# Optimization experiments

Measured on AMD Instinct MI355X. Metric: run time of the kernel, lower is better.

The kernel has to match this reference:

```python
import jax, jax.numpy as jnp
import numpy as np

N_EMBD = 1024

def setup_inputs() -> dict:
    key = jax.random.key(0)
    ks = jax.random.split(key, 7)
    x = jax.random.normal(ks[0], (4, 2048, N_EMBD), dtype=jnp.float32)
    s = 1.0 / np.sqrt(N_EMBD)
    Wk = jax.random.normal(ks[1], (N_EMBD, N_EMBD), dtype=jnp.float32) * s
    bk = jnp.zeros((N_EMBD,), dtype=jnp.float32)
    Wq = jax.random.normal(ks[2], (N_EMBD, N_EMBD), dtype=jnp.float32) * s
    bq = jnp.zeros((N_EMBD,), dtype=jnp.float32)
    Wv = jax.random.normal(ks[3], (N_EMBD, N_EMBD), dtype=jnp.float32) * s
    bv = jnp.zeros((N_EMBD,), dtype=jnp.float32)
    return {"x": x, "Wk": Wk, "bk": bk, "Wq": Wq, "bq": bq, "Wv": Wv, "bv": bv}

def reference(x, Wk, bk, Wq, bq, Wv, bv):
    B, T, C = x.shape
    k = x @ Wk.T + bk  # [B,T,C]
    q = x @ Wq.T + bq
    v = x @ Wv.T + bv
    # scaled scores with causal mask (note: original scales by C**-0.5)
    scores = jnp.einsum('btc,bsc->bts', q, k) * (C ** -0.5)  # [B,T,T]
    causal = jnp.tril(jnp.ones((T, T), dtype=bool))
    scores = jnp.where(causal, scores, -jnp.inf)
    weights = jax.nn.softmax(scores, axis=-1)
    # dropout disabled (inference mode)
    y = jnp.einsum('bts,bsc->btc', weights, v)
    return y
```

## Files before the change

kernel.cpp:

```cpp
#include <hip/hip_runtime.h>
#include <hip/hip_bf16.h>

typedef __attribute__((ext_vector_type(8))) short short8;
typedef __attribute__((ext_vector_type(4))) float f32x4;

__device__ __forceinline__ ushort f2b(float f) {
    __hip_bfloat16 h = __float2bfloat16(f);
    return *reinterpret_cast<ushort*>(&h);
}
__device__ __forceinline__ float b2f(ushort u) {
    return __uint_as_float(((unsigned)u) << 16);
}
__device__ __forceinline__ void gload16(const ushort* g, ushort* l) {
    __builtin_amdgcn_global_load_lds(
        (const __attribute__((address_space(1))) void*)g,
        (__attribute__((address_space(3))) void*)l, 16, 0, 0);
}

__global__ __launch_bounds__(512, 1) void qkv_gemm256(
    const ushort* __restrict__ xb, const ushort* __restrict__ Wcat,
    const float* __restrict__ bk, const float* __restrict__ bq, const float* __restrict__ bv,
    ushort* __restrict__ Kb, ushort* __restrict__ Qb, ushort* __restrict__ Vt) {
    constexpr int T = 2048, C = 1024, K = 1024, NT = 16;
    __shared__ ushort smem[49152];

    const int tid = threadIdx.x;
    const int l = tid & 63, w = tid >> 6;
    const int wm = (w >> 2) * 128, wn = (w & 3) * 32;
    const int lr = l & 15, lk = l >> 4;

    const int b = blockIdx.x;
    const int wg = (b & 7) * 96 + (b >> 3);
    const int m0 = (wg / 24) * 256, n0 = (wg % 24) * 128;

    const int srow = w * 16 + (l >> 2);
    const int scb = ((l & 3) << 4) ^ ((l & 32) ? 32 : 0);
    const ushort* gA = xb + (size_t)(m0 + srow) * K + (scb >> 1);
    const ushort* gB = Wcat + (size_t)(n0 + srow) * K + (scb >> 1);

    const int LB = lr * 32 + ((lk << 3) ^ ((lr >= 8) ? 16 : 0));

    f32x4 acc[8][2] = {};

#define STAGEQ(u1, ks)                                                    \
    {                                                                     \
        ushort* _base = smem + ((u1) & 1) * 24576 + (ks) * 12288;         \
        const int _ko = (u1) * 64 + (ks) * 32;                            \
        ushort* _da = _base + w * 512;                                    \
        gload16(gA + _ko, _da);                                           \
        gload16(gA + (size_t)128 * K + _ko, _da + 4096);                  \
        gload16(gB + _ko, _base + 8192 + w * 512);                        \
    }

    STAGEQ(0, 0);
    STAGEQ(0, 1);

    for (int u = 0; u < NT; ++u) {
        const ushort* buf = smem + (u & 1) * 24576;
        asm volatile("s_waitcnt vmcnt(3)" ::: "memory");
        __builtin_amdgcn_s_barrier();
        asm volatile("" ::: "memory");
        {
            const ushort* Ab = buf + (wm >> 4) * 512 + LB;
            const ushort* Bb = buf + 8192 + (wn >> 4) * 512 + LB;
            short8 a[8], bf2[2];
#pragma unroll
            for (int f = 0; f < 8; ++f) a[f] = *reinterpret_cast<const short8*>(Ab + f * 512);
            bf2[0] = *reinterpret_cast<const short8*>(Bb);
            bf2[1] = *reinterpret_cast<const short8*>(Bb + 512);
            if (u + 1 < NT) STAGEQ(u + 1, 0);
            __builtin_amdgcn_s_setprio(1);
#pragma unroll
            for (int f = 0; f < 8; ++f)
#pragma unroll
                for (int g = 0; g < 2; ++g)
                    acc[f][g] = __builtin_amdgcn_mfma_f32_16x16x32_bf16(a[f], bf2[g], acc[f][g], 0, 0, 0);
            __builtin_amdgcn_s_setprio(0);
        }
        if (u + 1 < NT) asm volatile("s_waitcnt vmcnt(3)" ::: "memory");
        else            asm volatile("s_waitcnt vmcnt(0)" ::: "memory");
        __builtin_amdgcn_s_barrier();
        asm volatile("" ::: "memory");
        {
            const ushort* Ab = buf + 12288 + (wm >> 4) * 512 + LB;
            const ushort* Bb = buf + 12288 + 8192 + (wn >> 4) * 512 + LB;
            short8 a[8], bf2[2];
#pragma unroll
            for (int f = 0; f < 8; ++f) a[f] = *reinterpret_cast<const short8*>(Ab + f * 512);
            bf2[0] = *reinterpret_cast<const short8*>(Bb);
            bf2[1] = *reinterpret_cast<const short8*>(Bb + 512);
            if (u + 1 < NT) STAGEQ(u + 1, 1);
            __builtin_amdgcn_s_setprio(1);
#pragma unroll
            for (int f = 0; f < 8; ++f)
#pragma unroll
                for (int g = 0; g < 2; ++g)
                    acc[f][g] = __builtin_amdgcn_mfma_f32_16x16x32_bf16(a[f], bf2[g], acc[f][g], 0, 0, 0);
            __builtin_amdgcn_s_setprio(0);
        }
    }
#undef STAGEQ

    const int zsel = n0 >> 10;
    const int c0 = (n0 & 1023) + wn;
    if (zsel < 2) {
        ushort* O = (zsel == 0) ? Kb : Qb;
        const float* bias = (zsel == 0) ? bk : bq;
#pragma unroll
        for (int f = 0; f < 8; ++f)
#pragma unroll
            for (int g = 0; g < 2; ++g) {
                const int gc = c0 + g * 16 + lr;
                const float badd = bias[gc];
#pragma unroll
                for (int rr = 0; rr < 4; ++rr) {
                    const int gr = m0 + wm + f * 16 + lk * 4 + rr;
                    O[(size_t)gr * C + gc] = f2b(acc[f][g][rr] + badd);
                }
            }
    } else {
        const int zb = (m0 + wm) >> 11;
        const int s0 = (m0 + wm) & 2047;
        ushort* Vz = Vt + (size_t)zb * C * T;
#pragma unroll
        for (int f = 0; f < 8; ++f)
#pragma unroll
            for (int g = 0; g < 2; ++g) {
                const int gc = c0 + g * 16 + lr;
                const float badd = bv[gc];
                const int s = s0 + f * 16 + lk * 4;
                ushort tmp[4];
#pragma unroll
                for (int rr = 0; rr < 4; ++rr) tmp[rr] = f2b(acc[f][g][rr] + badd);
                *reinterpret_cast<uint2*>(Vz + (size_t)gc * T + s) =
                    *reinterpret_cast<uint2*>(tmp);
            }
    }
}

template <int MODE>
__global__ __launch_bounds__(256, 3) void gemm_ring(
    const ushort* __restrict__ Kb, const ushort* __restrict__ Qb,
    const ushort* __restrict__ Vt, ushort* __restrict__ Sb, float* __restrict__ out) {
    constexpr int T = 2048, C = 1024;
    __shared__ ushort smem[24576];

    const int tid = threadIdx.x;
    const int l = tid & 63, w = tid >> 6;
    const int wm = (w >> 1) * 64, wn = (w & 1) * 64;
    const int lr = l & 15, lk = l >> 4;

    int m0, n0, nt, iblk = 0, jblk = 0, z = 0;
    const ushort *Au, *Bu;
    int ldA, ldB;
    if constexpr (MODE == 1) {
        const int wg0 = blockIdx.x;
        const int wg = (wg0 & 7) * 68 + (wg0 >> 3);
        z = wg / 136; const int t136 = wg % 136;
        int i = (int)((sqrtf(8.f * t136 + 1.f) - 1.f) * 0.5f);
        while ((i + 1) * (i + 2) / 2 <= t136) ++i;
        while (i * (i + 1) / 2 > t136) --i;
        const int j = t136 - i * (i + 1) / 2;
        iblk = i; jblk = j;
        m0 = i * 128; n0 = j * 128;
        Au = Qb + (size_t)z * T * C + (size_t)m0 * C; ldA = C;
        Bu = Kb + (size_t)z * T * C + (size_t)n0 * C; ldB = C;
        nt = 32;
    } else {
        const int wg0 = blockIdx.x;
        const int wg = (wg0 & 7) * 64 + (wg0 >> 3);
        const int half = wg >> 8, s2 = wg & 255;
        z = s2 >> 6; const int r6 = s2 & 63;
        const int nb = r6 & 7, ii = r6 >> 3;
        const int i = half ? (15 - ii) : ii;
        iblk = i;
        m0 = i * 128; n0 = nb * 128;
        Au = Sb + (size_t)z * T * T + (size_t)m0 * T; ldA = T;
        Bu = Vt + (size_t)z * C * T + (size_t)n0 * T; ldB = T;
        nt = 4 * (i + 1);
    }

    const int srow = w * 16 + (l >> 2);
    const int scb = ((l & 3) << 4) ^ ((l >= 32) ? 32 : 0);
    const ushort* gA = Au + (size_t)srow * ldA + (scb >> 1);
    const ushort* gB = Bu + (size_t)srow * ldB + (scb >> 1);
    const size_t a64 = (size_t)64 * ldA, b64 = (size_t)64 * ldB;
    const int LBu = lr * 32 + ((lk << 3) ^ ((lr >= 8) ? 16 : 0));

    f32x4 acc[4][4] = {};

#define STAGE(tt, sl)                                                    \
    {                                                                    \
        const int _ko = (tt) * 32;                                       \
        ushort* _d = smem + (sl) * 8192 + w * 512;                       \
        gload16(gA + _ko,        _d);                                    \
        gload16(gA + a64 + _ko,  _d + 2048);                             \
        gload16(gB + _ko,        _d + 4096);                             \
        gload16(gB + b64 + _ko,  _d + 6144);                             \
    }

    STAGE(0, 0);
    STAGE(1, 1);
    asm volatile("s_waitcnt vmcnt(4)" ::: "memory");
    __builtin_amdgcn_s_barrier();
    asm volatile("" ::: "memory");

    int sc = 0, ss = 2;
    for (int t = 0; t < nt; ++t) {
        const ushort* As = smem + sc * 8192 + (wm >> 4) * 512 + LBu;
        const ushort* Bs = smem + sc * 8192 + 4096 + (wn >> 4) * 512 + LBu;
        short8 af[4], bf[4];
#pragma unroll
        for (int q = 0; q < 4; ++q) {
            af[q] = *reinterpret_cast<const short8*>(As + q * 512);
            bf[q] = *reinterpret_cast<const short8*>(Bs + q * 512);
        }
        if (t + 2 < nt) STAGE(t + 2, ss);
        __builtin_amdgcn_s_setprio(1);
#pragma unroll
        for (int mf = 0; mf < 4; ++mf)
#pragma unroll
            for (int nf = 0; nf < 4; ++nf)
                acc[mf][nf] = __builtin_amdgcn_mfma_f32_16x16x32_bf16(af[mf], bf[nf], acc[mf][nf], 0, 0, 0);
        __builtin_amdgcn_s_setprio(0);
        if (t + 1 < nt) {
            if (t + 2 < nt) asm volatile("s_waitcnt vmcnt(4)" ::: "memory");
            else            asm volatile("s_waitcnt vmcnt(0)" ::: "memory");
            __builtin_amdgcn_s_barrier();
            asm volatile("" ::: "memory");
        }
        sc = (sc == 2) ? 0 : sc + 1;
        ss = (ss == 2) ? 0 : ss + 1;
    }
#undef STAGE

    if constexpr (MODE == 1) {
        ushort* Sp = Sb + (size_t)z * T * T;
        const bool diag = (iblk == jblk);
#pragma unroll
        for (int mf = 0; mf < 4; ++mf)
#pragma unroll
            for (int nf = 0; nf < 4; ++nf) {
                const int gc = n0 + wn + nf * 16 + lr;
#pragma unroll
                for (int rr = 0; rr < 4; ++rr) {
                    const int gr = m0 + wm + mf * 16 + lk * 4 + rr;
                    if (!diag || gc <= gr)
                        Sp[(size_t)gr * T + gc] = f2b(acc[mf][nf][rr] * 0.03125f);
                }
            }
    } else {
        float* Op = out + (size_t)z * T * C;
#pragma unroll
        for (int mf = 0; mf < 4; ++mf)
#pragma unroll
            for (int nf = 0; nf < 4; ++nf) {
                const int gc = n0 + wn + nf * 16 + lr;
#pragma unroll
                for (int rr = 0; rr < 4; ++rr) {
                    const int gr = m0 + wm + mf * 16 + lk * 4 + rr;
                    Op[(size_t)gr * C + gc] = acc[mf][nf][rr];
                }
            }
    }
}

__global__ __launch_bounds__(256) void cvt_all(
    const float* __restrict__ x, const float* __restrict__ Wk,
    const float* __restrict__ Wq, const float* __restrict__ Wv,
    ushort* __restrict__ xb, ushort* __restrict__ Wcat) {
    constexpr int C = 1024;
    constexpr int NX = 8388608 / 8, NW = C * C / 8;
    int i = blockIdx.x * 256 + threadIdx.x;
    const float* src; ushort* dst;
    if (i < NX)               { src = x;  dst = xb; }
    else if (i < NX + NW)     { src = Wk; dst = Wcat;                 i -= NX; }
    else if (i < NX + 2 * NW) { src = Wq; dst = Wcat + (size_t)C * C; i -= NX + NW; }
    else                      { src = Wv; dst = Wcat + 2 * (size_t)C * C; i -= NX + 2 * NW; }
    const float4* p = reinterpret_cast<const float4*>(src) + (size_t)i * 2;
    float4 a = p[0], b = p[1];
    ushort o[8] = {f2b(a.x), f2b(a.y), f2b(a.z), f2b(a.w),
                   f2b(b.x), f2b(b.y), f2b(b.z), f2b(b.w)};
    reinterpret_cast<uint4*>(dst)[i] = *reinterpret_cast<uint4*>(o);
}

__global__ __launch_bounds__(256) void softmax_rows(ushort* __restrict__ S, int T) {
    const int g = blockIdx.x;
    const int r = g & (T - 1);
    ushort* p = S + (size_t)g * T;
    const int tid = threadIdx.x;
    const int lane = tid & 63, wave = tid >> 6;
    const int c0 = tid * 8;
    const int n_write = ((r >> 7) + 1) << 7;

    float f[8];
    if (c0 <= r) {
        uint4 raw = *reinterpret_cast<const uint4*>(p + c0);
        ushort* rs = reinterpret_cast<ushort*>(&raw);
#pragma unroll
        for (int j = 0; j < 8; ++j) f[j] = (c0 + j <= r) ? b2f(rs[j]) : -INFINITY;
    } else {
#pragma unroll
        for (int j = 0; j < 8; ++j) f[j] = -INFINITY;
    }

    float mx = f[0];
#pragma unroll
    for (int j = 1; j < 8; ++j) mx = fmaxf(mx, f[j]);
#pragma unroll
    for (int o = 32; o > 0; o >>= 1) mx = fmaxf(mx, __shfl_xor(mx, o));

    __shared__ float redm[4], reds[4];
    if (lane == 0) redm[wave] = mx;
    __syncthreads();
    mx = fmaxf(fmaxf(redm[0], redm[1]), fmaxf(redm[2], redm[3]));

    float e[8], s = 0.f;
#pragma unroll
    for (int j = 0; j < 8; ++j) { e[j] = __expf(f[j] - mx); s += e[j]; }
#pragma unroll
    for (int o = 32; o > 0; o >>= 1) s += __shfl_xor(s, o);
    if (lane == 0) reds[wave] = s;
    __syncthreads();
    s = reds[0] + reds[1] + reds[2] + reds[3];

    const float inv = 1.f / s;
    if (c0 < n_write) {
        ushort outv[8];
#pragma unroll
        for (int j = 0; j < 8; ++j) outv[j] = f2b(e[j] * inv);
        *reinterpret_cast<uint4*>(p + c0) = *reinterpret_cast<uint4*>(outv);
    }
}

extern "C" void kernel_launch(void* const* d_in, const int* in_sizes, int n_in,
                              void* d_out, int out_size, void* d_ws, size_t ws_size,
                              hipStream_t stream) {
    const float* x  = (const float*)d_in[0];
    const float* Wk = (const float*)d_in[1];
    const float* bk = (const float*)d_in[2];
    const float* Wq = (const float*)d_in[3];
    const float* bq = (const float*)d_in[4];
    const float* Wv = (const float*)d_in[5];
    const float* bv = (const float*)d_in[6];
    float* out = (float*)d_out;

    constexpr int B = 4, T = 2048, C = 1024;
    constexpr size_t BTC = (size_t)B * T * C;

    ushort* Kb = (ushort*)d_ws;
    ushort* Qb = Kb + BTC;
    ushort* Vt = Qb + BTC;
    ushort* Sb = Vt + BTC;
    ushort* xb   = Sb;
    ushort* Wcat = Sb + BTC;

    dim3 blk(256);

    cvt_all<<<dim3(5632), blk, 0, stream>>>(x, Wk, Wq, Wv, xb, Wcat);

    qkv_gemm256<<<dim3(768), dim3(512), 0, stream>>>(xb, Wcat, bk, bq, bv, Kb, Qb, Vt);

    gemm_ring<1><<<dim3(544), blk, 0, stream>>>(Kb, Qb, Vt, Sb, out);

    softmax_rows<<<dim3(B * T), blk, 0, stream>>>(Sb, T);

    gemm_ring<2><<<dim3(512), blk, 0, stream>>>(Kb, Qb, Vt, Sb, out);
}
```

Before: 145.6 us.

## Enlarge QKV GEMM tile to 256x256 with 4-slot k32 LDS ring

```diff
diff --git a/kernel.cpp b/kernel.cpp
--- a/kernel.cpp
+++ b/kernel.cpp
@@ -21,17 +21,17 @@
     const ushort* __restrict__ xb, const ushort* __restrict__ Wcat,
     const float* __restrict__ bk, const float* __restrict__ bq, const float* __restrict__ bv,
     ushort* __restrict__ Kb, ushort* __restrict__ Qb, ushort* __restrict__ Vt) {
-    constexpr int T = 2048, C = 1024, K = 1024, NT = 16;
-    __shared__ ushort smem[49152];
+    constexpr int T = 2048, C = 1024, K = 1024, NT = 32;
+    __shared__ ushort smem[65536];
 
     const int tid = threadIdx.x;
     const int l = tid & 63, w = tid >> 6;
-    const int wm = (w >> 2) * 128, wn = (w & 3) * 32;
+    const int wm = (w >> 2) * 128, wn = (w & 3) * 64;
     const int lr = l & 15, lk = l >> 4;
 
     const int b = blockIdx.x;
-    const int wg = (b & 7) * 96 + (b >> 3);
-    const int m0 = (wg / 24) * 256, n0 = (wg % 24) * 128;
+    const int wg = (b & 7) * 48 + (b >> 3);
+    const int m0 = (wg / 12) * 256, n0 = (wg % 12) * 256;
 
     const int srow = w * 16 + (l >> 2);
     const int scb = ((l & 3) << 4) ^ ((l & 32) ? 32 : 0);
@@ -39,65 +39,49 @@
     const ushort* gB = Wcat + (size_t)(n0 + srow) * K + (scb >> 1);
 
     const int LB = lr * 32 + ((lk << 3) ^ ((lr >= 8) ? 16 : 0));
-
-    f32x4 acc[8][2] = {};
-
-#define STAGEQ(u1, ks)                                                    \
+    const int Abase = (wm >> 7) * 4096;
+    const int Bbase = 8192 + ((wn >> 7) * 4096) + ((wn & 64) >> 4) * 512;
+
+    f32x4 acc[8][4] = {};
+
+#define STAGEQ(tt)                                                        \
     {                                                                     \
-        ushort* _base = smem + ((u1) & 1) * 24576 + (ks) * 12288;         \
-        const int _ko = (u1) * 64 + (ks) * 32;                            \
-        ushort* _da = _base + w * 512;                                    \
-        gload16(gA + _ko, _da);                                           \
-        gload16(gA + (size_t)128 * K + _ko, _da + 4096);                  \
-        gload16(gB + _ko, _base + 8192 + w * 512);                        \
-    }
-
-    STAGEQ(0, 0);
-    STAGEQ(0, 1);
+        const int _ko = (tt) * 32;                                        \
+        ushort* _s = smem + ((tt) & 3) * 16384 + w * 512;                 \
+        gload16(gA + _ko,                  _s);                           \
+        gload16(gA + (size_t)128 * K + _ko, _s + 4096);                   \
+        gload16(gB + _ko,                  _s + 8192);                    \
+        gload16(gB + (size_t)128 * K + _ko, _s + 12288);                  \
+    }
+
+    STAGEQ(0); STAGEQ(1); STAGEQ(2);
 
     for (int u = 0; u < NT; ++u) {
-        const ushort* buf = smem + (u & 1) * 24576;
-        asm volatile("s_waitcnt vmcnt(3)" ::: "memory");
+        const int rem = NT - 1 - u;
+        if (rem >= 2)      asm volatile("s_waitcnt vmcnt(8)" ::: "memory");
+        else if (rem == 1) asm volatile("s_waitcnt vmcnt(4)" ::: "memory");
+        else               asm volatile("s_waitcnt vmcnt(0)" ::: "memory");
         __builtin_amdgcn_s_barrier();
         asm volatile("" ::: "memory");
-        {
-            const ushort* Ab = buf + (wm >> 4) * 512 + LB;
-            const ushort* Bb = buf + 8192 + (wn >> 4) * 512 + LB;
-            short8 a[8], bf2[2];
-#pragma unroll
-            for (int f = 0; f < 8; ++f) a[f] = *reinterpret_cast<const short8*>(Ab + f * 512);
-            bf2[0] = *reinterpret_cast<const short8*>(Bb);
-            bf2[1] = *reinterpret_cast<const short8*>(Bb + 512);
-            if (u + 1 < NT) STAGEQ(u + 1, 0);
-            __builtin_amdgcn_s_setprio(1);
-#pragma unroll
-            for (int f = 0; f < 8; ++f)
-#pragma unroll
-                for (int g = 0; g < 2; ++g)
-                    acc[f][g] = __builtin_amdgcn_mfma_f32_16x16x32_bf16(a[f], bf2[g], acc[f][g], 0, 0, 0);
-            __builtin_amdgcn_s_setprio(0);
-        }
-        if (u + 1 < NT) asm volatile("s_waitcnt vmcnt(3)" ::: "memory");
-        else            asm volatile("s_waitcnt vmcnt(0)" ::: "memory");
-        __builtin_amdgcn_s_barrier();
-        asm volatile("" ::: "memory");
-        {
-            const ushort* Ab = buf + 12288 + (wm >> 4) * 512 + LB;
-            const ushort* Bb = buf + 12288 + 8192 + (wn >> 4) * 512 + LB;
-            short8 a[8], bf2[2];
-#pragma unroll
-            for (int f = 0; f < 8; ++f) a[f] = *reinterpret_cast<const short8*>(Ab + f * 512);
-            bf2[0] = *reinterpret_cast<const short8*>(Bb);
-            bf2[1] = *reinterpret_cast<const short8*>(Bb + 512);
-            if (u + 1 < NT) STAGEQ(u + 1, 1);
-            __builtin_amdgcn_s_setprio(1);
-#pragma unroll
-            for (int f = 0; f < 8; ++f)
-#pragma unroll
-                for (int g = 0; g < 2; ++g)
-                    acc[f][g] = __builtin_amdgcn_mfma_f32_16x16x32_bf16(a[f], bf2[g], acc[f][g], 0, 0, 0);
-            __builtin_amdgcn_s_setprio(0);
-        }
+
+        const ushort* slot = smem + (u & 3) * 16384;
+        const ushort* Ab = slot + Abase + LB;
+        const ushort* Bb = slot + Bbase + LB;
+        short8 af[8], bfr[4];
+#pragma unroll
+        for (int f = 0; f < 8; ++f) af[f] = *reinterpret_cast<const short8*>(Ab + f * 512);
+#pragma unroll
+        for (int g = 0; g < 4; ++g) bfr[g] = *reinterpret_cast<const short8*>(Bb + g * 512);
+
+        if (u + 3 < NT) STAGEQ(u + 3);
+
+        __builtin_amdgcn_s_setprio(1);
+#pragma unroll
+        for (int f = 0; f < 8; ++f)
+#pragma unroll
+            for (int g = 0; g < 4; ++g)
+                acc[f][g] = __builtin_amdgcn_mfma_f32_16x16x32_bf16(af[f], bfr[g], acc[f][g], 0, 0, 0);
+        __builtin_amdgcn_s_setprio(0);
     }
 #undef STAGEQ
 
@@ -109,7 +93,7 @@
 #pragma unroll
         for (int f = 0; f < 8; ++f)
 #pragma unroll
-            for (int g = 0; g < 2; ++g) {
+            for (int g = 0; g < 4; ++g) {
                 const int gc = c0 + g * 16 + lr;
                 const float badd = bias[gc];
 #pragma unroll
@@ -125,7 +109,7 @@
 #pragma unroll
         for (int f = 0; f < 8; ++f)
 #pragma unroll
-            for (int g = 0; g < 2; ++g) {
+            for (int g = 0; g < 4; ++g) {
                 const int gc = c0 + g * 16 + lr;
                 const float badd = bv[gc];
                 const int s = s0 + f * 16 + lk * 4;
@@ -359,7 +343,7 @@
 
     cvt_all<<<dim3(5632), blk, 0, stream>>>(x, Wk, Wq, Wv, xb, Wcat);
 
-    qkv_gemm256<<<dim3(768), dim3(512), 0, stream>>>(xb, Wcat, bk, bq, bv, Kb, Qb, Vt);
+    qkv_gemm256<<<dim3(384), dim3(512), 0, stream>>>(xb, Wcat, bk, bq, bv, Kb, Qb, Vt);
 
     gemm_ring<1><<<dim3(544), blk, 0, stream>>>(Kb, Qb, Vt, Sb, out);
 
```

After: 154.1 us. 1.06x slower.
